# Optimization experiments

Measured on AMD Instinct MI355X. Metric: run time of the kernel, lower is better.

The kernel has to match this reference:

```python
import jax, jax.numpy as jnp
import numpy as np

N = 65536        # query points per chunk
V = 512          # latent shape vertices
K = 8            # cdist top-k
H = 512          # hidden dim
NB = 4           # num blocks
NL = 2           # extra hidden layers per block
F0 = (V + 1) * 3 + 3 * K   # 1563 first-block input features
FI = F0 + H                # 2075 later-block input features (skip concat)


def setup_inputs() -> dict:
    key = jax.random.key(0)
    ks = jax.random.split(key, 6)
    s = 0.02  # small weight scale to keep tanh unsaturated
    return {
        "cxyz": jax.random.normal(ks[0], (N, 3 + 3 * V), dtype=jnp.float32),
        "W_first": jax.random.normal(ks[1], (F0, H), dtype=jnp.float32) * s,
        "b_first": jnp.zeros((H,), jnp.float32),
        "W_in": jax.random.normal(ks[2], (NB - 1, FI, H), dtype=jnp.float32) * s,
        "b_in": jnp.zeros((NB - 1, H), jnp.float32),
        "W_hidden": jax.random.normal(ks[3], (NB, NL, H, H), dtype=jnp.float32) * s,
        "b_hidden": jnp.zeros((NB, NL, H), jnp.float32),
        "W_out": jax.random.normal(ks[4], (H, 1), dtype=jnp.float32) * s,
        "b_out": jnp.zeros((1,), jnp.float32),
    }


def _forward(cxyz, W_first, b_first, W_in, b_in, W_hidden, b_hidden, W_out, b_out):
    xyz = cxyz[:, :3]                       # [N, 3]
    latent = cxyz[:, 3:]                    # [N, 3V]
    lat3 = latent.reshape(latent.shape[0], -1, 3)  # [N, V, 3]

    # kNN retrieval: squared euclidean distances give identical top-k indices
    # to torch.cdist (sqrt is monotone); we only use the indices.
    d2 = jnp.sum((xyz[:, None, :] - lat3) ** 2, axis=-1)   # [N, V]
    _, idx = jax.lax.top_k(-d2, K)                          # smallest-K indices [N, K]
    sel = jnp.take_along_axis(lat3, idx[:, :, None], axis=1)  # [N, K, 3]

    xyz_aug = jnp.concatenate([xyz, sel.reshape(sel.shape[0], -1)], axis=1)  # [N, 3+3K]
    x_ = jnp.concatenate([xyz_aug, latent], axis=1)                          # [N, F0]

    relu = jax.nn.relu
    # block 0
    x = relu(x_ @ W_first + b_first)
    for l in range(NL):
        x = relu(x @ W_hidden[0, l] + b_hidden[0, l])
    # blocks 1..NB-1 with skip concat of x_
    for b in range(1, NB):
        x = jnp.concatenate([x, x_], axis=1)   # [N, FI]
        x = relu(x @ W_in[b - 1] + b_in[b - 1])
        for l in range(NL):
            x = relu(x @ W_hidden[b, l] + b_hidden[b, l])
    return jnp.tanh(x @ W_out + b_out)          # [N, 1]


def reference(cxyz, W_first, b_first, W_in, b_in, W_hidden, b_hidden, W_out, b_out):
    return _forward(cxyz, W_first, b_first, W_in, b_in, W_hidden, b_hidden, W_out, b_out)
```

## Files before the change

kernel.cpp:

```cpp
#include <hip/hip_runtime.h>

typedef unsigned short u16;
typedef _Float16 f16;
typedef __attribute__((ext_vector_type(8))) _Float16 f16x8;
typedef __attribute__((ext_vector_type(4))) float f32x4;

#define NPTS 65536

__device__ __forceinline__ u16 f2h(float f) {
    f16 h = (f16)f;
    return __builtin_bit_cast(u16, h);
}

__device__ __forceinline__ unsigned pack2(float a, float b) {
    return (unsigned)f2h(a) | ((unsigned)f2h(b) << 16);
}

__device__ __forceinline__ void async_copy16(const u16* g, u16* l) {
    __builtin_amdgcn_global_load_lds(
        (const __attribute__((address_space(1))) void*)g,
        (__attribute__((address_space(3))) void*)l, 16, 0, 0);
}

__global__ __launch_bounds__(256) void knn_kernel(const float* __restrict__ cxyz,
                                                  u16* __restrict__ xpad) {
#pragma clang fp contract(off)
    const int lane = threadIdx.x & 63;
    const int wave = threadIdx.x >> 6;
    const size_t p = (size_t)blockIdx.x * 4 + wave;
    const float* row = cxyz + p * 1539;
    u16* orow = xpad + p * 1568;

    float vals[24];
    const float* lp = row + 3 + lane * 24;
#pragma unroll
    for (int i = 0; i < 24; ++i) vals[i] = lp[i];

    float x0 = row[0], y0 = row[1], z0 = row[2];

    unsigned long long cand[8];
#pragma unroll
    for (int t = 0; t < 8; ++t) {
        float dx = x0 - vals[3 * t + 0];
        float dy = y0 - vals[3 * t + 1];
        float dz = z0 - vals[3 * t + 2];
        float d2 = dx * dx + dy * dy;
        d2 = d2 + dz * dz;
        cand[t] = (((unsigned long long)__float_as_uint(d2)) << 32) |
                  (unsigned)(lane * 8 + t);
    }

    for (int r = 0; r < 8; ++r) {
        unsigned long long m = cand[0];
#pragma unroll
        for (int t = 1; t < 8; ++t) m = (cand[t] < m) ? cand[t] : m;
#pragma unroll
        for (int o = 1; o < 64; o <<= 1) {
            unsigned long long o2 = __shfl_xor(m, o, 64);
            m = (o2 < m) ? o2 : m;
        }
#pragma unroll
        for (int t = 0; t < 8; ++t)
            if (cand[t] == m) cand[t] = ~0ULL;
        if (lane == r) {
            unsigned jw = (unsigned)m;
            orow[3 + 3 * r + 0] = f2h(row[3 + 3 * jw + 0]);
            orow[3 + 3 * r + 1] = f2h(row[3 + 3 * jw + 1]);
            orow[3 + 3 * r + 2] = f2h(row[3 + 3 * jw + 2]);
        }
    }

    if (lane < 3) orow[lane] = f2h(row[lane]);
    if (lane >= 27 && lane < 32) orow[lane] = 0;

    unsigned w[12];
#pragma unroll
    for (int i = 0; i < 12; ++i) w[i] = pack2(vals[2 * i], vals[2 * i + 1]);
    uint4* op = (uint4*)(orow + 32 + lane * 24);
    op[0] = make_uint4(w[0], w[1], w[2], w[3]);
    op[1] = make_uint4(w[4], w[5], w[6], w[7]);
    op[2] = make_uint4(w[8], w[9], w[10], w[11]);
}

__global__ __launch_bounds__(256) void prep_w1(const float* __restrict__ Wf,
                                               u16* __restrict__ W1p) {
    int idx = blockIdx.x * 256 + threadIdx.x;
    if (idx >= 512 * 1568) return;
    int n = idx / 1568, kp = idx % 1568;
    float v = 0.f;
    if (kp < 27) v = Wf[(size_t)kp * 512 + n];
    else if (kp >= 32) v = Wf[(size_t)(kp - 5) * 512 + n];
    W1p[idx] = f2h(v);
}

__global__ __launch_bounds__(256) void prep_win(const float* __restrict__ Win,
                                                u16* __restrict__ Winp) {
    int idx = blockIdx.x * 256 + threadIdx.x;
    if (idx >= 3 * 512 * 2080) return;
    int b = idx / (512 * 2080);
    int r = idx % (512 * 2080);
    int n = r / 2080, kp = r % 2080;
    float v = 0.f;
    if (kp < 539) v = Win[((size_t)b * 2075 + kp) * 512 + n];
    else if (kp >= 544) v = Win[((size_t)b * 2075 + kp - 5) * 512 + n];
    Winp[idx] = f2h(v);
}

__global__ __launch_bounds__(256) void prep_wh(const float* __restrict__ Wh,
                                               u16* __restrict__ Whp) {
    int idx = blockIdx.x * 256 + threadIdx.x;
    if (idx >= 8 * 512 * 512) return;
    int m = idx / (512 * 512);
    int r = idx % (512 * 512);
    int n = r / 512, k = r % 512;
    Whp[idx] = f2h(Wh[((size_t)m * 512 + k) * 512 + n]);
}

__global__ __launch_bounds__(256, 4) void gemm_f16(
    const u16* __restrict__ A0, int ld0, int kt0,
    const u16* __restrict__ A1, int ld1, int kt1,
    const u16* __restrict__ B,
    const float* __restrict__ bias,
    u16* __restrict__ C,
    int mb8) {
    __shared__ u16 As[2][128 * 32];
    __shared__ u16 Bs[2][128 * 32];
    const int tid = threadIdx.x;
    const int lane = tid & 63;
    const int wave = tid >> 6;
    const int ktot = kt0 + kt1;
    const size_t ldB = (size_t)ktot * 32;

    const int bid = blockIdx.x;
    const int idx = bid >> 3;
    const int mb = (bid & 7) * mb8 + (idx >> 2);
    const int nb = idx & 3;
    const size_t mbase = (size_t)mb * 128;
    const int nbase = nb * 128;

    f32x4 acc[4][4];
#pragma unroll
    for (int i = 0; i < 4; ++i)
#pragma unroll
        for (int j = 0; j < 4; ++j) acc[i][j] = (f32x4){0.f, 0.f, 0.f, 0.f};

    const int r4 = lane >> 2;
    const int c8 = (lane & 3) * 8;
    const size_t arow0 = mbase + wave * 32 + r4;
    const size_t brow0 = (size_t)nbase + wave * 32 + r4;

    const int m0 = (wave & 1) * 64;
    const int n0 = (wave >> 1) * 64;
    const int rowsel = lane & 15;
    const int quad8 = (lane >> 4) * 8;

    auto stage = [&](int t, int b) {
        u16* lA0 = &As[b][(wave * 32 + 0) * 32];
        u16* lA1 = &As[b][(wave * 32 + 16) * 32];
        u16* lB0 = &Bs[b][(wave * 32 + 0) * 32];
        u16* lB1 = &Bs[b][(wave * 32 + 16) * 32];
        if (t < kt0) {
            const size_t off = arow0 * (size_t)ld0 + t * 32 + c8;
            async_copy16(A0 + off, lA0);
            async_copy16(A0 + off + 16 * (size_t)ld0, lA1);
        } else {
            const size_t off = arow0 * (size_t)ld1 + (t - kt0) * 32 + c8;
            async_copy16(A1 + off, lA0);
            async_copy16(A1 + off + 16 * (size_t)ld1, lA1);
        }
        const size_t boff = brow0 * ldB + t * 32 + c8;
        async_copy16(B + boff, lB0);
        async_copy16(B + boff + 16 * ldB, lB1);
    };

    stage(0, 0);
    __syncthreads();

    int cur = 0;
    for (int t = 0; t < ktot; ++t) {
        if (t + 1 < ktot) stage(t + 1, cur ^ 1);

        f16x8 af[4], bfr[4];
#pragma unroll
        for (int i = 0; i < 4; ++i) {
            af[i]  = __builtin_bit_cast(f16x8, *(const uint4*)&As[cur][(m0 + i * 16 + rowsel) * 32 + quad8]);
            bfr[i] = __builtin_bit_cast(f16x8, *(const uint4*)&Bs[cur][(n0 + i * 16 + rowsel) * 32 + quad8]);
        }
#pragma unroll
        for (int i = 0; i < 4; ++i)
#pragma unroll
            for (int j = 0; j < 4; ++j)
                acc[i][j] = __builtin_amdgcn_mfma_f32_16x16x32_f16(
                    af[i], bfr[j], acc[i][j], 0, 0, 0);

        __syncthreads();
        cur ^= 1;
    }

#pragma unroll
    for (int j = 0; j < 4; ++j) {
        const int col = nbase + n0 + j * 16 + (lane & 15);
        const float bv = bias[col];
#pragma unroll
        for (int i = 0; i < 4; ++i) {
#pragma unroll
            for (int r = 0; r < 4; ++r) {
                const size_t rowg = mbase + m0 + i * 16 + (lane >> 4) * 4 + r;
                float v = acc[i][j][r] + bv;
                v = v > 0.f ? v : 0.f;
                C[rowg * 512 + col] = f2h(v);
            }
        }
    }
}

__global__ __launch_bounds__(256) void out_kernel(const u16* __restrict__ x,
                                                  const float* __restrict__ Wout,
                                                  const float* __restrict__ bout,
                                                  float* __restrict__ out) {
    const int lane = threadIdx.x & 63;
    const int wave = threadIdx.x >> 6;
    const size_t p = (size_t)blockIdx.x * 4 + wave;
    uint4 xv = *(const uint4*)(x + p * 512 + lane * 8);
    const f16* xs = (const f16*)&xv;
    float s = 0.f;
#pragma unroll
    for (int i = 0; i < 8; ++i) s += (float)xs[i] * Wout[lane * 8 + i];
#pragma unroll
    for (int o = 1; o < 64; o <<= 1) s += __shfl_xor(s, o, 64);
    if (lane == 0) out[p] = tanhf(s + bout[0]);
}

extern "C" void kernel_launch(void* const* d_in, const int* in_sizes, int n_in,
                              void* d_out, int out_size, void* d_ws, size_t ws_size,
                              hipStream_t stream) {
    const float* cxyz = (const float*)d_in[0];
    const float* Wf   = (const float*)d_in[1];
    const float* bf   = (const float*)d_in[2];
    const float* Win  = (const float*)d_in[3];
    const float* bin  = (const float*)d_in[4];
    const float* Wh   = (const float*)d_in[5];
    const float* bh   = (const float*)d_in[6];
    const float* Wout = (const float*)d_in[7];
    const float* bout = (const float*)d_in[8];
    float* out = (float*)d_out;
    u16* wsb = (u16*)d_ws;

    const size_t N = NPTS;
    u16* xpad = wsb;
    u16* xa   = xpad + N * 1568;
    u16* xb   = xa + N * 512;
    u16* W1p  = xb + N * 512;
    u16* Winp = W1p + (size_t)512 * 1568;
    u16* Whp  = Winp + (size_t)3 * 512 * 2080;

    knn_kernel<<<dim3(N / 4), dim3(256), 0, stream>>>(cxyz, xpad);

    prep_w1<<<dim3((512 * 1568 + 255) / 256), dim3(256), 0, stream>>>(Wf, W1p);
    prep_win<<<dim3((3 * 512 * 2080 + 255) / 256), dim3(256), 0, stream>>>(Win, Winp);
    prep_wh<<<dim3((8 * 512 * 512 + 255) / 256), dim3(256), 0, stream>>>(Wh, Whp);

    const int MB8 = (int)(N / 128) / 8;
    const dim3 gg((N / 128) * 4), gb(256);
    const size_t WH = (size_t)512 * 512;
    const size_t WI = (size_t)512 * 2080;

    gemm_f16<<<gg, gb, 0, stream>>>(xpad, 1568, 49, nullptr, 0, 0, W1p, bf, xa, MB8);
    gemm_f16<<<gg, gb, 0, stream>>>(xa, 512, 16, nullptr, 0, 0, Whp + 0 * WH, bh + 0 * 512, xb, MB8);
    gemm_f16<<<gg, gb, 0, stream>>>(xb, 512, 16, nullptr, 0, 0, Whp + 1 * WH, bh + 1 * 512, xa, MB8);

    gemm_f16<<<gg, gb, 0, stream>>>(xa, 512, 16, xpad, 1568, 49, Winp + 0 * WI, bin + 0 * 512, xb, MB8);
    gemm_f16<<<gg, gb, 0, stream>>>(xb, 512, 16, nullptr, 0, 0, Whp + 2 * WH, bh + 2 * 512, xa, MB8);
    gemm_f16<<<gg, gb, 0, stream>>>(xa, 512, 16, nullptr, 0, 0, Whp + 3 * WH, bh + 3 * 512, xb, MB8);

    gemm_f16<<<gg, gb, 0, stream>>>(xb, 512, 16, xpad, 1568, 49, Winp + 1 * WI, bin + 1 * 512, xa, MB8);
    gemm_f16<<<gg, gb, 0, stream>>>(xa, 512, 16, nullptr, 0, 0, Whp + 4 * WH, bh + 4 * 512, xb, MB8);
    gemm_f16<<<gg, gb, 0, stream>>>(xb, 512, 16, nullptr, 0, 0, Whp + 5 * WH, bh + 5 * 512, xa, MB8);

    gemm_f16<<<gg, gb, 0, stream>>>(xa, 512, 16, xpad, 1568, 49, Winp + 2 * WI, bin + 2 * 512, xb, MB8);
    gemm_f16<<<gg, gb, 0, stream>>>(xb, 512, 16, nullptr, 0, 0, Whp + 6 * WH, bh + 6 * 512, xa, MB8);
    gemm_f16<<<gg, gb, 0, stream>>>(xa, 512, 16, nullptr, 0, 0, Whp + 7 * WH, bh + 7 * 512, xb, MB8);

    out_kernel<<<dim3(N / 4), dim3(256), 0, stream>>>(xb, Wout, bout, out);
}
```

Measured before the change: 1.768 ms.

## Triple-buffer GEMM LDS staging with XOR swizzle and single barrier per k-step

Moves the f16 GEMM from double-buffered to triple-buffered LDS, prefetching two k-tiles ahead. Each step uses an explicit vmcnt wait plus one barrier instead of a trailing __syncthreads. Global-to-LDS column offsets and LDS read offsets are XOR-swizzled to reduce bank conflicts, and s_setprio raises wave priority around the MFMA block. The goal is to hide global load latency and reduce LDS conflicts. In exchange, LDS per block grows by half and the occupancy hint drops from 4 to 3 blocks per CU.

```diff
diff --git a/kernel.cpp b/kernel.cpp
--- a/kernel.cpp
+++ b/kernel.cpp
@@ -116,15 +116,15 @@
     Whp[idx] = f2h(Wh[((size_t)m * 512 + k) * 512 + n]);
 }
 
-__global__ __launch_bounds__(256, 4) void gemm_f16(
+__global__ __launch_bounds__(256, 3) void gemm_f16(
     const u16* __restrict__ A0, int ld0, int kt0,
     const u16* __restrict__ A1, int ld1, int kt1,
     const u16* __restrict__ B,
     const float* __restrict__ bias,
     u16* __restrict__ C,
     int mb8) {
-    __shared__ u16 As[2][128 * 32];
-    __shared__ u16 Bs[2][128 * 32];
+    __shared__ u16 As[3][128 * 32];
+    __shared__ u16 Bs[3][128 * 32];
     const int tid = threadIdx.x;
     const int lane = tid & 63;
     const int wave = tid >> 6;
@@ -145,14 +145,14 @@
         for (int j = 0; j < 4; ++j) acc[i][j] = (f32x4){0.f, 0.f, 0.f, 0.f};
 
     const int r4 = lane >> 2;
-    const int c8 = (lane & 3) * 8;
+    const int c8s = (((lane & 3) ^ ((lane >> 3) & 3)) * 8);
     const size_t arow0 = mbase + wave * 32 + r4;
     const size_t brow0 = (size_t)nbase + wave * 32 + r4;
 
     const int m0 = (wave & 1) * 64;
     const int n0 = (wave >> 1) * 64;
     const int rowsel = lane & 15;
-    const int quad8 = (lane >> 4) * 8;
+    const int colrd = (((lane >> 4) ^ ((rowsel >> 1) & 3)) * 8);
 
     auto stage = [&](int t, int b) {
         u16* lA0 = &As[b][(wave * 32 + 0) * 32];
@@ -160,41 +160,47 @@
         u16* lB0 = &Bs[b][(wave * 32 + 0) * 32];
         u16* lB1 = &Bs[b][(wave * 32 + 16) * 32];
         if (t < kt0) {
-            const size_t off = arow0 * (size_t)ld0 + t * 32 + c8;
+            const size_t off = arow0 * (size_t)ld0 + t * 32 + c8s;
             async_copy16(A0 + off, lA0);
             async_copy16(A0 + off + 16 * (size_t)ld0, lA1);
         } else {
-            const size_t off = arow0 * (size_t)ld1 + (t - kt0) * 32 + c8;
+            const size_t off = arow0 * (size_t)ld1 + (t - kt0) * 32 + c8s;
             async_copy16(A1 + off, lA0);
             async_copy16(A1 + off + 16 * (size_t)ld1, lA1);
         }
-        const size_t boff = brow0 * ldB + t * 32 + c8;
+        const size_t boff = brow0 * ldB + t * 32 + c8s;
         async_copy16(B + boff, lB0);
         async_copy16(B + boff + 16 * ldB, lB1);
     };
 
     stage(0, 0);
-    __syncthreads();
-
-    int cur = 0;
+    if (1 < ktot) stage(1, 1);
+
     for (int t = 0; t < ktot; ++t) {
-        if (t + 1 < ktot) stage(t + 1, cur ^ 1);
+        const int cb = t % 3;
+        if (t + 1 < ktot) {
+            asm volatile("s_waitcnt vmcnt(4)" ::: "memory");
+        } else {
+            asm volatile("s_waitcnt vmcnt(0)" ::: "memory");
+        }
+        __builtin_amdgcn_s_barrier();
+        __builtin_amdgcn_sched_barrier(0);
+        if (t + 2 < ktot) stage(t + 2, (t + 2) % 3);
 
         f16x8 af[4], bfr[4];
 #pragma unroll
         for (int i = 0; i < 4; ++i) {
-            af[i]  = __builtin_bit_cast(f16x8, *(const uint4*)&As[cur][(m0 + i * 16 + rowsel) * 32 + quad8]);
-            bfr[i] = __builtin_bit_cast(f16x8, *(const uint4*)&Bs[cur][(n0 + i * 16 + rowsel) * 32 + quad8]);
-        }
+            af[i]  = __builtin_bit_cast(f16x8, *(const uint4*)&As[cb][(m0 + i * 16 + rowsel) * 32 + colrd]);
+            bfr[i] = __builtin_bit_cast(f16x8, *(const uint4*)&Bs[cb][(n0 + i * 16 + rowsel) * 32 + colrd]);
+        }
+        __builtin_amdgcn_s_setprio(1);
 #pragma unroll
         for (int i = 0; i < 4; ++i)
 #pragma unroll
             for (int j = 0; j < 4; ++j)
                 acc[i][j] = __builtin_amdgcn_mfma_f32_16x16x32_f16(
                     af[i], bfr[j], acc[i][j], 0, 0, 0);
-
-        __syncthreads();
-        cur ^= 1;
+        __builtin_amdgcn_s_setprio(0);
     }
 
 #pragma unroll
```

Measured after the change: 1.887 ms. 6.7% more time.
